# Performance work log

Measured on AMD Instinct MI355X. Metric: run time of the kernel, lower is better.

## Reference

```python
import jax, jax.numpy as jnp
import numpy as np

EPS = 1e-06
N_HEADS = 16


def elu_feature_map(x):
    return jax.nn.elu(x) + 1.0


def setup_inputs() -> dict:
    key = jax.random.key(0)
    ks = jax.random.split(key, 5)
    B, S, D = 4, 4096, 1024
    scale = 1.0 / np.sqrt(D)
    x = jax.random.normal(ks[0], (B, S, D), dtype=jnp.float32)
    Wq = jax.random.normal(ks[1], (D, D), dtype=jnp.float32) * scale
    Wk = jax.random.normal(ks[2], (D, D), dtype=jnp.float32) * scale
    Wv = jax.random.normal(ks[3], (D, D), dtype=jnp.float32) * scale
    Wo = jax.random.normal(ks[4], (D, D), dtype=jnp.float32) * scale
    return {"x": x, "Wq": Wq, "Wk": Wk, "Wv": Wv, "Wo": Wo}


def reference(x, Wq, Wk, Wv, Wo):
    B, S, D = x.shape
    H = N_HEADS
    hd = D // H
    # nn.Linear(bias=False): y = x @ W.T
    q = (x @ Wq.T).reshape(B, S, H, hd)
    k = (x @ Wk.T).reshape(B, S, H, hd)
    v = (x @ Wv.T).reshape(B, S, H, hd)
    q = elu_feature_map(q)
    k = elu_feature_map(k)
    KV = jnp.einsum('bshd,bshe->bhde', k, v)          # [B,H,hd,hd]
    out = jnp.einsum('bshd,bhde->bshe', q, KV)        # [B,S,H,hd]
    k_sum = k.sum(axis=1)                             # [B,H,hd]
    z = jnp.einsum('bshd,bhd->bsh', q, k_sum)[..., None]
    out = out / (z + EPS)
    out = out.reshape(B, S, D)
    return out @ Wo.T
```

## Files before the change

### kernel.cpp

```cpp
#include <hip/hip_runtime.h>
#include <hip/hip_bf16.h>

#define BB 4
#define SS 4096
#define DD 1024
#define HH 16
#define HD 64
#define MM (BB * SS)
#define KK DD
#define NN DD

typedef __bf16 bf16x8 __attribute__((ext_vector_type(8)));
typedef float f32x4 __attribute__((ext_vector_type(4)));

typedef __attribute__((address_space(3))) void lds_void_t;
typedef const __attribute__((address_space(1))) void glb_void_t;

__global__ __launch_bounds__(256)
void cvt_all(const float* __restrict__ x,
             const float* __restrict__ wq, const float* __restrict__ wk,
             const float* __restrict__ wv, const float* __restrict__ wo,
             __hip_bfloat16* __restrict__ base)
{
    const int blk = blockIdx.x;
    const float* src;
    __hip_bfloat16* dst;
    int i;
    if (blk < (MM * KK / 1024)) {
        src = x;
        dst = base;
        i = blk * 256 + threadIdx.x;
    } else {
        const int r = blk - (MM * KK / 1024);
        const int w = r >> 10;
        src = (w == 0) ? wq : (w == 1) ? wk : (w == 2) ? wv : wo;
        dst = base + (size_t)(MM * KK) + (size_t)w * (NN * KK);
        i = (r & 1023) * 256 + threadIdx.x;
    }
    float4 v = ((const float4*)src)[i];
    union { __hip_bfloat16 h[4]; uint2 u; } p;
    p.h[0] = __float2bfloat16(v.x);
    p.h[1] = __float2bfloat16(v.y);
    p.h[2] = __float2bfloat16(v.z);
    p.h[3] = __float2bfloat16(v.w);
    ((uint2*)dst)[i] = p.u;
}

#define RD_A(dst, idx)                                                                   \
    dst[0] = *(const bf16x8*)(sAb + ((idx) * 16 + lr) * 128 + ((lq * 16) ^ swz));        \
    dst[1] = *(const bf16x8*)(sAb + ((idx) * 16 + lr) * 128 + (((64) + lq * 16) ^ swz));

#define MFMA2(i0, i1, va, vb)                                                                         \
    __builtin_amdgcn_s_setprio(1);                                                                    \
    _Pragma("unroll")                                                                                 \
    for (int j = 0; j < 4; ++j) {                                                                     \
        acc[i0][j] = __builtin_amdgcn_mfma_f32_16x16x32_bf16(va[0], bfr[j][0], acc[i0][j], 0, 0, 0);  \
        acc[i0][j] = __builtin_amdgcn_mfma_f32_16x16x32_bf16(va[1], bfr[j][1], acc[i0][j], 0, 0, 0);  \
        acc[i1][j] = __builtin_amdgcn_mfma_f32_16x16x32_bf16(vb[0], bfr[j][0], acc[i1][j], 0, 0, 0);  \
        acc[i1][j] = __builtin_amdgcn_mfma_f32_16x16x32_bf16(vb[1], bfr[j][1], acc[i1][j], 0, 0, 0);  \
    }                                                                                                 \
    __builtin_amdgcn_s_setprio(0);

template<int MODE>
__global__ __launch_bounds__(512, 2)
void gemm256(const __hip_bfloat16* __restrict__ Ain,
             const __hip_bfloat16* __restrict__ Bin,
             __hip_bfloat16* __restrict__ Obf,
             float* __restrict__ Of32)
{
    __shared__ __align__(16) __hip_bfloat16 sA[2][2][128 * 64];
    __shared__ __align__(16) __hip_bfloat16 sB[2][2][128 * 64];

    const int bid = blockIdx.x;
    const int mt  = ((bid & 7) << 3) | ((bid >> 3) & 7);
    const int nt  = bid >> 6;
    const int m0  = mt << 8;
    const int n0  = nt << 8;

    const int t      = threadIdx.x;
    const int lane   = t & 63;
    const int w      = t >> 6;
    const int warp_m = w >> 2;
    const int warp_n = w & 3;
    const int halfB  = warp_n >> 1;
    const int bn     = (warp_n & 1) << 6;
    const int lr     = lane & 15;
    const int lq     = lane >> 4;
    const int swz    = (lr & 7) << 4;

    const int trow = t >> 3;
    const int tcb  = (((t & 7) ^ ((t >> 3) & 7)) << 4);

    auto stage = [&](int ht) {
        if (ht >= 64) return;
        const int ts   = ht >> 2;
        const int kind = ht & 3;
        const int half = kind & 1;
        #pragma unroll
        for (int i = 0; i < 2; ++i) {
            const int row = i * 64 + trow;
            if (kind >= 2) {
                __builtin_amdgcn_global_load_lds(
                    (glb_void_t*)(Ain + (size_t)(m0 + half * 128 + row) * 1024 + ts * 64 + (tcb >> 1)),
                    (lds_void_t*)(&sA[ts & 1][half][(i * 512 + t) * 8]), 16, 0, 0);
            } else {
                __builtin_amdgcn_global_load_lds(
                    (glb_void_t*)(Bin + (size_t)(n0 + half * 128 + row) * 1024 + ts * 64 + (tcb >> 1)),
                    (lds_void_t*)(&sB[ts & 1][half][(i * 512 + t) * 8]), 16, 0, 0);
            }
        }
    };

    f32x4 acc[8][4];
    #pragma unroll
    for (int i = 0; i < 8; ++i)
        #pragma unroll
        for (int j = 0; j < 4; ++j)
            acc[i][j] = (f32x4){0.f, 0.f, 0.f, 0.f};

    stage(0); stage(1); stage(2); stage(3);
    stage(4); stage(5); stage(6);
    asm volatile("s_waitcnt vmcnt(6)" ::: "memory");
    __builtin_amdgcn_s_barrier();

    #pragma unroll 2
    for (int kt = 0; kt < 16; ++kt) {
        const char* sAb = (const char*)&sA[kt & 1][warp_m][0];
        const char* sBb = (const char*)&sB[kt & 1][halfB][0];
        bf16x8 bfr[4][2];
        bf16x8 a0[2], a1[2], a2[2], a3[2], a4[2], a5[2], a6[2], a7[2];

        #pragma unroll
        for (int j = 0; j < 4; ++j) {
            bfr[j][0] = *(const bf16x8*)(sBb + (bn + j * 16 + lr) * 128 + ((lq * 16) ^ swz));
            bfr[j][1] = *(const bf16x8*)(sBb + (bn + j * 16 + lr) * 128 + ((64 + lq * 16) ^ swz));
        }
        RD_A(a0, 0); RD_A(a1, 1);
        RD_A(a2, 2); RD_A(a3, 3);
        stage(4 * kt + 7);

        asm volatile("s_waitcnt lgkmcnt(4)" ::: "memory");
        __builtin_amdgcn_sched_barrier(0);
        MFMA2(0, 1, a0, a1);
        RD_A(a4, 4); RD_A(a5, 5);
        RD_A(a6, 6); RD_A(a7, 7);

        asm volatile("s_waitcnt lgkmcnt(8)" ::: "memory");
        __builtin_amdgcn_sched_barrier(0);
        MFMA2(2, 3, a2, a3);
        __builtin_amdgcn_s_barrier();
        stage(4 * kt + 8);
        stage(4 * kt + 9);

        asm volatile("s_waitcnt lgkmcnt(4)" ::: "memory");
        __builtin_amdgcn_sched_barrier(0);
        MFMA2(4, 5, a4, a5);
        asm volatile("s_waitcnt lgkmcnt(0)" ::: "memory");
        __builtin_amdgcn_sched_barrier(0);
        MFMA2(6, 7, a6, a7);
        __builtin_amdgcn_s_barrier();
        stage(4 * kt + 10);

        if (kt < 14)       { asm volatile("s_waitcnt vmcnt(6)" ::: "memory"); }
        else if (kt == 14) { asm volatile("s_waitcnt vmcnt(0)" ::: "memory"); }
        __builtin_amdgcn_s_barrier();
    }

    if constexpr (MODE == 0) {
        const int wsel = n0 >> 10;
        const int nb   = n0 & 1023;
        __hip_bfloat16* Op = Obf + (size_t)wsel * ((size_t)MM * KK);
        if (wsel == 0) {
            #pragma unroll
            for (int i = 0; i < 8; ++i)
                #pragma unroll
                for (int j = 0; j < 4; ++j)
                    #pragma unroll
                    for (int r = 0; r < 4; ++r) {
                        const int row = m0 + warp_m * 128 + i * 16 + lq * 4 + r;
                        const int col = nb + warp_n * 64 + j * 16 + lr;
                        float v = acc[i][j][r];
                        v = (v > 0.f) ? v + 1.f : __expf(v);
                        Op[(size_t)row * 1024 + col] = __float2bfloat16(v);
                    }
        } else {
            const bool doelu = (wsel == 1);
            #pragma unroll
            for (int i = 0; i < 8; ++i)
                #pragma unroll
                for (int j = 0; j < 4; ++j) {
                    const int row0 = m0 + warp_m * 128 + i * 16 + lq * 4;
                    const int col  = nb + warp_n * 64 + j * 16 + lr;
                    const int b    = row0 >> 12;
                    const int s    = row0 & 4095;
                    union { __hip_bfloat16 hh[4]; uint2 u; } pk;
                    #pragma unroll
                    for (int r = 0; r < 4; ++r) {
                        float v = acc[i][j][r];
                        if (doelu) v = (v > 0.f) ? v + 1.f : __expf(v);
                        pk.hh[r] = __float2bfloat16(v);
                    }
                    *(uint2*)(Op + ((size_t)((b * 16 + (col >> 6)) * 64 + (col & 63)) * 4096 + s)) = pk.u;
                }
        }
    } else {
        #pragma unroll
        for (int i = 0; i < 8; ++i)
            #pragma unroll
            for (int j = 0; j < 4; ++j)
                #pragma unroll
                for (int r = 0; r < 4; ++r) {
                    const int row = m0 + warp_m * 128 + i * 16 + lq * 4 + r;
                    const int col = n0 + warp_n * 64 + j * 16 + lr;
                    Of32[(size_t)row * 1024 + col] = acc[i][j][r];
                }
    }
}

#define KV_SPLIT 8
__global__ __launch_bounds__(256)
void kv_gemm(const __hip_bfloat16* __restrict__ KB,
             const __hip_bfloat16* __restrict__ VB,
             float* __restrict__ KVp)
{
    __shared__ float sRed[65 * 66];

    const int bh = blockIdx.x;
    const int sp = blockIdx.y;
    const int t  = threadIdx.x;
    const int lane = t & 63;
    const int wv = t >> 6;
    const int lr = lane & 15;
    const int lq = lane >> 4;

    const __hip_bfloat16* kbase = KB + (size_t)bh * 64 * 4096;
    const __hip_bfloat16* vbase = VB + (size_t)bh * 64 * 4096;
    const int k0w = sp * 512 + wv * 128 + lq * 8;

    f32x4 acc[4][4];
    f32x4 ksacc[4];
    #pragma unroll
    for (int i = 0; i < 4; i++) {
        ksacc[i] = (f32x4){0.f, 0.f, 0.f, 0.f};
        #pragma unroll
        for (int j = 0; j < 4; j++)
            acc[i][j] = (f32x4){0.f, 0.f, 0.f, 0.f};
    }

    bf16x8 ones;
    #pragma unroll
    for (int j = 0; j < 8; j++) ones[j] = (__bf16)1.0f;

    #pragma unroll
    for (int c = 0; c < 4; ++c) {
        const int k0 = k0w + c * 32;
        bf16x8 ak[4], bv[4];
        #pragma unroll
        for (int i = 0; i < 4; ++i) {
            ak[i] = *(const bf16x8*)(kbase + (size_t)(i * 16 + lr) * 4096 + k0);
            bv[i] = *(const bf16x8*)(vbase + (size_t)(i * 16 + lr) * 4096 + k0);
        }
        #pragma unroll
        for (int i = 0; i < 4; ++i) {
            #pragma unroll
            for (int j = 0; j < 4; ++j)
                acc[i][j] = __builtin_amdgcn_mfma_f32_16x16x32_bf16(ak[i], bv[j], acc[i][j], 0, 0, 0);
            ksacc[i] = __builtin_amdgcn_mfma_f32_16x16x32_bf16(ak[i], ones, ksacc[i], 0, 0, 0);
        }
    }

    for (int w = 0; w < 4; w++) {
        if (wv == w) {
            #pragma unroll
            for (int i = 0; i < 4; i++) {
                #pragma unroll
                for (int j = 0; j < 4; j++) {
                    float* p = &sRed[(j * 16 + lr) * 66 + i * 16 + lq * 4];
                    if (w == 0) {
                        #pragma unroll
                        for (int r = 0; r < 4; r++) p[r] = acc[i][j][r];
                    } else {
                        #pragma unroll
                        for (int r = 0; r < 4; r++) p[r] += acc[i][j][r];
                    }
                }
                if (lr == 0) {
                    float* p = &sRed[64 * 66 + i * 16 + lq * 4];
                    if (w == 0) {
                        #pragma unroll
                        for (int r = 0; r < 4; r++) p[r] = ksacc[i][r];
                    } else {
                        #pragma unroll
                        for (int r = 0; r < 4; r++) p[r] += ksacc[i][r];
                    }
                }
            }
        }
        __syncthreads();
    }

    float* outp = KVp + (size_t)(sp * 64 + bh) * (65 * 64);
    #pragma unroll
    for (int i = 0; i < 17; i++) {
        int idx = i * 256 + t;
        if (idx < 65 * 64) {
            int e = idx >> 6, d = idx & 63;
            outp[idx] = sRed[e * 66 + d];
        }
    }
}

__global__ __launch_bounds__(256)
void kv_reduce(const float* __restrict__ KVp,
               __hip_bfloat16* __restrict__ KVt,
               float* __restrict__ KS)
{
    const int bh = blockIdx.x;
    const int t  = threadIdx.x;
    #pragma unroll
    for (int i = 0; i < 16; i++) {
        int idx = i * 256 + t;
        float s = 0.f;
        #pragma unroll
        for (int sp = 0; sp < KV_SPLIT; sp++)
            s += KVp[((size_t)(sp * 64 + bh) * 65) * 64 + idx];
        KVt[(size_t)bh * 4096 + idx] = __float2bfloat16(s);
    }
    if (t < 64) {
        float s = 0.f;
        #pragma unroll
        for (int sp = 0; sp < KV_SPLIT; sp++)
            s += KVp[((size_t)(sp * 64 + bh) * 65 + 64) * 64 + t];
        KS[bh * 64 + t] = s;
    }
}

__global__ __launch_bounds__(256)
void attn_mfma(const __hip_bfloat16* __restrict__ Q,
               const __hip_bfloat16* __restrict__ KVt,
               const float* __restrict__ KS,
               __hip_bfloat16* __restrict__ O)
{
    const int bh = blockIdx.x;
    const int b  = bh >> 4;
    const int h  = bh & 15;
    const int s0 = blockIdx.y * 128;
    const int t  = threadIdx.x;
    const int lane = t & 63;
    const int wv = t >> 6;

    __shared__ __align__(16) __hip_bfloat16 sQ[128][72];
    __shared__ __align__(16) __hip_bfloat16 sKVt[64][72];
    __shared__ float sKS[64];
    __shared__ float sZ[128];

    {
        const float4* kvp = (const float4*)(KVt + (size_t)bh * 4096);
        #pragma unroll
        for (int i = 0; i < 2; i++) {
            int c = i * 256 + t;
            *(float4*)(&sKVt[c >> 3][(c & 7) * 8]) = kvp[c];
        }
        if (t < 64) sKS[t] = KS[bh * 64 + t];
    }
    {
        const __hip_bfloat16* qp = Q + ((size_t)b * SS + s0) * DD + h * HD;
        int r  = t >> 1;
        int c0 = (t & 1) * 32;
        #pragma unroll
        for (int i = 0; i < 32; i += 8)
            *(float4*)(&sQ[r][c0 + i]) = *(const float4*)(qp + (size_t)r * DD + c0 + i);
    }
    __syncthreads();

    if (t < 128) {
        float z = 0.f;
        #pragma unroll
        for (int d8 = 0; d8 < 64; d8 += 8) {
            bf16x8 qv = *(const bf16x8*)(&sQ[t][d8]);
            #pragma unroll
            for (int j = 0; j < 8; j++) z += (float)qv[j] * sKS[d8 + j];
        }
        sZ[t] = 1.f / (z + 1e-6f);
    }

    const int lr = lane & 15;
    const int lq = lane >> 4;
    f32x4 acc[2][4];
    #pragma unroll
    for (int i = 0; i < 2; i++)
        #pragma unroll
        for (int j = 0; j < 4; j++)
            acc[i][j] = (f32x4){0.f, 0.f, 0.f, 0.f};

    bf16x8 af[2][2], bfv[4][2];
    #pragma unroll
    for (int ks = 0; ks < 2; ks++) {
        #pragma unroll
        for (int i = 0; i < 2; i++)
            af[i][ks] = *(const bf16x8*)(&sQ[wv * 32 + i * 16 + lr][lq * 8 + ks * 32]);
        #pragma unroll
        for (int j = 0; j < 4; j++)
            bfv[j][ks] = *(const bf16x8*)(&sKVt[j * 16 + lr][lq * 8 + ks * 32]);
    }
    #pragma unroll
    for (int i = 0; i < 2; i++)
        #pragma unroll
        for (int j = 0; j < 4; j++) {
            acc[i][j] = __builtin_amdgcn_mfma_f32_16x16x32_bf16(af[i][0], bfv[j][0], acc[i][j], 0, 0, 0);
            acc[i][j] = __builtin_amdgcn_mfma_f32_16x16x32_bf16(af[i][1], bfv[j][1], acc[i][j], 0, 0, 0);
        }
    __syncthreads();

    __hip_bfloat16* op = O + ((size_t)b * SS + s0) * DD + h * HD;
    #pragma unroll
    for (int i = 0; i < 2; i++)
        #pragma unroll
        for (int j = 0; j < 4; j++)
            #pragma unroll
            for (int r = 0; r < 4; r++) {
                int row = wv * 32 + i * 16 + lq * 4 + r;
                int col = j * 16 + lr;
                op[(size_t)row * DD + col] = __float2bfloat16(acc[i][j][r] * sZ[row]);
            }
}

extern "C" void kernel_launch(void* const* d_in, const int* in_sizes, int n_in,
                              void* d_out, int out_size, void* d_ws, size_t ws_size,
                              hipStream_t stream) {
    const float* x  = (const float*)d_in[0];
    const float* Wq = (const float*)d_in[1];
    const float* Wk = (const float*)d_in[2];
    const float* Wv = (const float*)d_in[3];
    const float* Wo = (const float*)d_in[4];
    float* out = (float*)d_out;

    char* ws = (char*)d_ws;
    const size_t XB_BYTES = (size_t)MM * KK * 2;
    const size_t WB_BYTES = (size_t)NN * KK * 2;
    __hip_bfloat16* xb  = (__hip_bfloat16*)(ws);
    __hip_bfloat16* wqb = (__hip_bfloat16*)(ws + XB_BYTES);
    __hip_bfloat16* wob = (__hip_bfloat16*)(ws + XB_BYTES + 3 * WB_BYTES);
    __hip_bfloat16* qb  = (__hip_bfloat16*)(ws + XB_BYTES + 4 * WB_BYTES);
    __hip_bfloat16* kb  = (__hip_bfloat16*)(ws + 2 * XB_BYTES + 4 * WB_BYTES);
    __hip_bfloat16* vb  = (__hip_bfloat16*)(ws + 3 * XB_BYTES + 4 * WB_BYTES);
    __hip_bfloat16* KVt = (__hip_bfloat16*)(ws + 4 * XB_BYTES + 4 * WB_BYTES);
    float*          KS  = (float*)(ws + 4 * XB_BYTES + 4 * WB_BYTES + 524288);
    float* KVp = (float*)(ws);
    __hip_bfloat16* ab = xb;

    cvt_all<<<(MM * KK + 4 * NN * KK) / 1024, 256, 0, stream>>>(x, Wq, Wk, Wv, Wo, xb);

    gemm256<0><<<768, 512, 0, stream>>>(xb, wqb, qb, nullptr);

    kv_gemm<<<dim3(BB * HH, KV_SPLIT), 256, 0, stream>>>(kb, vb, KVp);
    kv_reduce<<<BB * HH, 256, 0, stream>>>(KVp, KVt, KS);

    attn_mfma<<<dim3(BB * HH, SS / 128), 256, 0, stream>>>(qb, KVt, KS, ab);

    gemm256<1><<<256, 512, 0, stream>>>(ab, wob, nullptr, out);
}
```

Before: 324.8 us.

## Restructure GEMM main loop into barrier-fenced phases and split kv_reduce grid

The GEMM inner loop now runs four phases. Each phase loads two A fragments into a reused register pair, issues one async global-to-LDS stage, and waits at a barrier before its MFMAs. The prefetch depth drops from seven stages to six and A-fragment register use falls, which may help occupancy or scheduling, but the extra barriers and the lgkmcnt(0) waits in every phase can reduce overlap. Separately, kv_reduce is split across four blocks per head so more CUs share that small reduction.

```diff
diff --git a/kernel.cpp b/kernel.cpp
--- a/kernel.cpp
+++ b/kernel.cpp
@@ -61,6 +61,11 @@
     }                                                                                                 \
     __builtin_amdgcn_s_setprio(0);
 
+#define PH_ENTER                                                \
+    __builtin_amdgcn_s_barrier();                               \
+    asm volatile("s_waitcnt lgkmcnt(0)" ::: "memory");          \
+    __builtin_amdgcn_sched_barrier(0);
+
 template<int MODE>
 __global__ __launch_bounds__(512, 2)
 void gemm256(const __hip_bfloat16* __restrict__ Ain,
@@ -119,8 +124,8 @@
             acc[i][j] = (f32x4){0.f, 0.f, 0.f, 0.f};
 
     stage(0); stage(1); stage(2); stage(3);
-    stage(4); stage(5); stage(6);
-    asm volatile("s_waitcnt vmcnt(6)" ::: "memory");
+    stage(4); stage(5);
+    asm volatile("s_waitcnt vmcnt(4)" ::: "memory");
     __builtin_amdgcn_s_barrier();
 
     #pragma unroll 2
@@ -128,40 +133,37 @@
         const char* sAb = (const char*)&sA[kt & 1][warp_m][0];
         const char* sBb = (const char*)&sB[kt & 1][halfB][0];
         bf16x8 bfr[4][2];
-        bf16x8 a0[2], a1[2], a2[2], a3[2], a4[2], a5[2], a6[2], a7[2];
+        bf16x8 x0[2], x1[2];
 
         #pragma unroll
         for (int j = 0; j < 4; ++j) {
             bfr[j][0] = *(const bf16x8*)(sBb + (bn + j * 16 + lr) * 128 + ((lq * 16) ^ swz));
             bfr[j][1] = *(const bf16x8*)(sBb + (bn + j * 16 + lr) * 128 + ((64 + lq * 16) ^ swz));
         }
-        RD_A(a0, 0); RD_A(a1, 1);
-        RD_A(a2, 2); RD_A(a3, 3);
-        stage(4 * kt + 7);
-
-        asm volatile("s_waitcnt lgkmcnt(4)" ::: "memory");
-        __builtin_amdgcn_sched_barrier(0);
-        MFMA2(0, 1, a0, a1);
-        RD_A(a4, 4); RD_A(a5, 5);
-        RD_A(a6, 6); RD_A(a7, 7);
-
+        RD_A(x0, 0); RD_A(x1, 1);
+        stage(4 * (kt + 1) + 2);
         asm volatile("s_waitcnt lgkmcnt(8)" ::: "memory");
-        __builtin_amdgcn_sched_barrier(0);
-        MFMA2(2, 3, a2, a3);
+        PH_ENTER;
+        MFMA2(0, 1, x0, x1);
         __builtin_amdgcn_s_barrier();
-        stage(4 * kt + 8);
-        stage(4 * kt + 9);
-
-        asm volatile("s_waitcnt lgkmcnt(4)" ::: "memory");
-        __builtin_amdgcn_sched_barrier(0);
-        MFMA2(4, 5, a4, a5);
-        asm volatile("s_waitcnt lgkmcnt(0)" ::: "memory");
-        __builtin_amdgcn_sched_barrier(0);
-        MFMA2(6, 7, a6, a7);
+
+        RD_A(x0, 2); RD_A(x1, 3);
+        stage(4 * (kt + 1) + 3);
+        PH_ENTER;
+        MFMA2(2, 3, x0, x1);
         __builtin_amdgcn_s_barrier();
-        stage(4 * kt + 10);
-
-        if (kt < 14)       { asm volatile("s_waitcnt vmcnt(6)" ::: "memory"); }
+
+        RD_A(x0, 4); RD_A(x1, 5);
+        stage(4 * (kt + 2) + 0);
+        PH_ENTER;
+        MFMA2(4, 5, x0, x1);
+        __builtin_amdgcn_s_barrier();
+
+        RD_A(x0, 6); RD_A(x1, 7);
+        stage(4 * (kt + 2) + 1);
+        PH_ENTER;
+        MFMA2(6, 7, x0, x1);
+        if (kt < 14)       { asm volatile("s_waitcnt vmcnt(4)" ::: "memory"); }
         else if (kt == 14) { asm volatile("s_waitcnt vmcnt(0)" ::: "memory"); }
         __builtin_amdgcn_s_barrier();
     }
@@ -316,17 +318,18 @@
                float* __restrict__ KS)
 {
     const int bh = blockIdx.x;
+    const int q  = blockIdx.y;
     const int t  = threadIdx.x;
     #pragma unroll
-    for (int i = 0; i < 16; i++) {
-        int idx = i * 256 + t;
+    for (int i = 0; i < 4; i++) {
+        int idx = q * 1024 + i * 256 + t;
         float s = 0.f;
         #pragma unroll
         for (int sp = 0; sp < KV_SPLIT; sp++)
             s += KVp[((size_t)(sp * 64 + bh) * 65) * 64 + idx];
         KVt[(size_t)bh * 4096 + idx] = __float2bfloat16(s);
     }
-    if (t < 64) {
+    if (q == 0 && t < 64) {
         float s = 0.f;
         #pragma unroll
         for (int sp = 0; sp < KV_SPLIT; sp++)
@@ -454,7 +457,7 @@
     gemm256<0><<<768, 512, 0, stream>>>(xb, wqb, qb, nullptr);
 
     kv_gemm<<<dim3(BB * HH, KV_SPLIT), 256, 0, stream>>>(kb, vb, KVp);
-    kv_reduce<<<BB * HH, 256, 0, stream>>>(KVp, KVt, KS);
+    kv_reduce<<<dim3(BB * HH, 4), 256, 0, stream>>>(KVp, KVt, KS);
 
     attn_mfma<<<dim3(BB * HH, SS / 128), 256, 0, stream>>>(qb, KVt, KS, ab);
 
```

Result: faster. 301.7 us (-7.1%).
